# Optimization experiments

Measured on AMD Instinct MI355X. Metric: run time of the kernel, lower is better.

The kernel has to match this reference:

```python
import jax, jax.numpy as jnp
import numpy as np

# Single-directional chamfer distance (pytorch3d semantics):
# chamfer_distance(x, y, single_directional=True) returns
# (mean over batch of mean over points of min_j ||x_i - y_j||^2, None)
# Here forward(v, v_pred) = chamfer_distance(v_pred, v, single_directional=True)

CHUNK = 1024  # tile size over query points to avoid materializing full [B,N,M]

def _min_sqdist(x, y):
    # x: [B, N, 3] queries, y: [B, M, 3] targets
    # returns [B, N] min squared distances, computed in chunks over N
    B, N, D = x.shape
    y_sq = jnp.sum(y * y, axis=-1)  # [B, M]

    def chunk_min(x_chunk):
        # x_chunk: [B, C, 3]
        x_sq = jnp.sum(x_chunk * x_chunk, axis=-1)  # [B, C]
        xy = jnp.einsum('bcd,bmd->bcm', x_chunk, y)  # [B, C, M]
        d2 = x_sq[:, :, None] - 2.0 * xy + y_sq[:, None, :]
        return jnp.min(d2, axis=-1)  # [B, C]

    n_chunks = N // CHUNK
    xr = x.reshape(B, n_chunks, CHUNK, D).transpose(1, 0, 2, 3)  # [n_chunks, B, C, 3]
    mins = jax.lax.map(chunk_min, xr)  # [n_chunks, B, C]
    return mins.transpose(1, 0, 2).reshape(B, N)


def setup_inputs() -> dict:
    key = jax.random.key(0)
    k1, k2 = jax.random.split(key)
    v = jax.random.normal(k1, (8, 16384, 3), dtype=jnp.float32)
    v_pred = jax.random.normal(k2, (8, 16384, 3), dtype=jnp.float32)
    return {"v": v, "v_pred": v_pred}


def reference(v, v_pred):
    # chamfer_distance(v_pred, v, single_directional=True)
    min_d2 = _min_sqdist(v_pred, v)  # [B, N]
    # pytorch3d default: sum over points per cloud, normalize by num points,
    # then mean-reduce over batch (batch_reduction='mean', point_reduction='mean')
    per_cloud = jnp.mean(min_d2, axis=-1)  # [B]
    loss = jnp.sum(per_cloud) / v_pred.shape[0]
    return loss
```

## Files before the change

### kernel.cpp

```cpp
#include <hip/hip_runtime.h>


typedef _Float16 half8 __attribute__((ext_vector_type(8)));
typedef float   f32x16 __attribute__((ext_vector_type(16)));

#define BB 8
#define NN 16384
#define MM 16384
#define THREADS 256
#define WAVES   (THREADS / 64)
#define QT 2
#define Q_PER_BLOCK (WAVES * QT * 32)
#define QC_SPLIT (NN / Q_PER_BLOCK)
#define PASS_TILES 64
#define PASS_TGT  (PASS_TILES * 32)
#define NPASS     (MM / PASS_TGT)

__device__ inline float min3f(float a, float b, float c) {
    return fminf(fminf(a, b), c);
}
__device__ inline float fold16(const f32x16 c, float r) {
    const float t0 = min3f(c[0],  c[1],  c[2]);
    const float t1 = min3f(c[3],  c[4],  c[5]);
    const float t2 = min3f(c[6],  c[7],  c[8]);
    const float t3 = min3f(c[9],  c[10], c[11]);
    const float t4 = min3f(c[12], c[13], c[14]);
    return min3f(min3f(t0, t1, t2), min3f(t3, t4, c[15]), r);
}

__global__ __launch_bounds__(THREADS, 2)
void chamfer_kernel(const float* __restrict__ v,
                    const float* __restrict__ vp,
                    float* __restrict__ out)
{
    __shared__ half8 shA[PASS_TILES * 64];

    const int tid  = threadIdx.x;
    const int lane = tid & 63;
    const int l31  = lane & 31;
    const int hi   = lane >> 5;
    const int wav  = tid >> 6;

    const int bx = blockIdx.x;
    const int qc = bx & (QC_SPLIT - 1);
    const int b  = bx >> 6;

    const float* vb = v  + (size_t)b * MM * 3;
    const float* vq = vp + (size_t)b * NN * 3;

    half8 b0, b1;
    float x20, x21;
    {
        const int qt0 = (qc * Q_PER_BLOCK) / 32 + wav * QT;
#pragma unroll
        for (int j = 0; j < QT; ++j) {
            const int q = (qt0 + j) * 32 + l31;
            const float x = vq[q*3+0], y = vq[q*3+1], z = vq[q*3+2];
            const float hx = (float)(_Float16)x; const float lx = x - hx;
            const float hy = (float)(_Float16)y; const float ly = y - hy;
            const float hz = (float)(_Float16)z; const float lz = z - hz;
            const float x2 = x*x + y*y + z*z;
            half8 t_;
            if (hi == 0) {
                t_[0] = (_Float16)hx; t_[1] = (_Float16)hy; t_[2] = (_Float16)hz;
                t_[3] = (_Float16)(32.f * lx);
                t_[4] = (_Float16)(32.f * ly);
                t_[5] = (_Float16)(32.f * lz);
                t_[6] = (_Float16)(0.03125f * hx);
                t_[7] = (_Float16)(0.03125f * hy);
            } else {
                t_[0] = (_Float16)(0.03125f * hz);
                t_[1] = (_Float16)1.f;
                t_[2] = (_Float16)0.03125f;
                t_[3] = (_Float16)0.f; t_[4] = (_Float16)0.f;
                t_[5] = (_Float16)0.f; t_[6] = (_Float16)0.f; t_[7] = (_Float16)0.f;
            }
            if (j == 0) { b0 = t_; x20 = x2; } else { b1 = t_; x21 = x2; }
        }
    }

    f32x16 Z;
#pragma unroll
    for (int e = 0; e < 16; ++e) Z[e] = 0.f;

    float r0 = 3.4e38f, r1 = 3.4e38f;

    for (int pass = 0; pass < NPASS; ++pass) {
        __syncthreads();
#pragma unroll
        for (int k = 0; k < 8; ++k) {
            const int tl = tid + k * THREADS;
            const int t  = pass * PASS_TGT + tl;
            const float yx = vb[t*3+0], yy = vb[t*3+1], yz = vb[t*3+2];
            const float hx = (float)(_Float16)yx; const float lx = yx - hx;
            const float hy = (float)(_Float16)yy; const float ly = yy - hy;
            const float hz = (float)(_Float16)yz; const float lz = yz - hz;
            const float y2 = yx*yx + yy*yy + yz*yz;
            const float h2 = (float)(_Float16)y2; const float l2 = y2 - h2;
            half8 f0, f1;
            f0[0] = (_Float16)(-2.f     * hx);
            f0[1] = (_Float16)(-2.f     * hy);
            f0[2] = (_Float16)(-2.f     * hz);
            f0[3] = (_Float16)(-0.0625f * hx);
            f0[4] = (_Float16)(-0.0625f * hy);
            f0[5] = (_Float16)(-0.0625f * hz);
            f0[6] = (_Float16)(-64.f    * lx);
            f0[7] = (_Float16)(-64.f    * ly);
            f1[0] = (_Float16)(-64.f    * lz);
            f1[1] = (_Float16)h2;
            f1[2] = (_Float16)(32.f     * l2);
            f1[3] = (_Float16)0.f; f1[4] = (_Float16)0.f;
            f1[5] = (_Float16)0.f; f1[6] = (_Float16)0.f; f1[7] = (_Float16)0.f;
            const int tile = tl >> 5, l = tl & 31;
            shA[tile * 64 + l]      = f0;
            shA[tile * 64 + 32 + l] = f1;
        }
        __syncthreads();

        half8 fA = shA[0 * 64 + lane];
        f32x16 cA0 = __builtin_amdgcn_mfma_f32_32x32x16_f16(fA, b0, Z, 0, 0, 0);
        f32x16 cA1 = __builtin_amdgcn_mfma_f32_32x32x16_f16(fA, b1, Z, 0, 0, 0);
        half8 fB = shA[1 * 64 + lane];

        for (int tt = 0; tt < PASS_TILES - 2; tt += 2) {
            fA = shA[(tt + 2) * 64 + lane];
            const f32x16 cB0 = __builtin_amdgcn_mfma_f32_32x32x16_f16(fB, b0, Z, 0, 0, 0);
            const f32x16 cB1 = __builtin_amdgcn_mfma_f32_32x32x16_f16(fB, b1, Z, 0, 0, 0);
            r0 = fold16(cA0, r0);
            r1 = fold16(cA1, r1);
            fB = shA[(tt + 3) * 64 + lane];
            cA0 = __builtin_amdgcn_mfma_f32_32x32x16_f16(fA, b0, Z, 0, 0, 0);
            cA1 = __builtin_amdgcn_mfma_f32_32x32x16_f16(fA, b1, Z, 0, 0, 0);
            r0 = fold16(cB0, r0);
            r1 = fold16(cB1, r1);
        }
        const f32x16 cB0 = __builtin_amdgcn_mfma_f32_32x32x16_f16(fB, b0, Z, 0, 0, 0);
        const f32x16 cB1 = __builtin_amdgcn_mfma_f32_32x32x16_f16(fB, b1, Z, 0, 0, 0);
        r0 = fold16(cA0, r0);
        r1 = fold16(cA1, r1);
        r0 = fold16(cB0, r0);
        r1 = fold16(cB1, r1);
    }

    const float m0 = fminf(r0, __shfl_xor(r0, 32, 64));
    const float m1 = fminf(r1, __shfl_xor(r1, 32, 64));
    const float d0 = fmaxf(m0 + x20, 0.f);
    const float d1 = fmaxf(m1 + x21, 0.f);
    float s = (hi == 0) ? (d0 + d1) : 0.f;
#pragma unroll
    for (int off = 32; off; off >>= 1) s += __shfl_down(s, off, 64);

    __syncthreads();
    float* fs = (float*)shA;
    if (lane == 0) fs[wav] = s;
    __syncthreads();
    if (tid == 0) {
        const float t = fs[0] + fs[1] + fs[2] + fs[3];
        atomicAdd(out, t * (1.0f / ((float)BB * (float)NN)));
    }
}

extern "C" void kernel_launch(void* const* d_in, const int* in_sizes, int n_in,
                              void* d_out, int out_size, void* d_ws, size_t ws_size,
                              hipStream_t stream) {
    const float* v  = (const float*)d_in[0];
    const float* vp = (const float*)d_in[1];
    float* out = (float*)d_out;

    hipMemsetAsync(out, 0, sizeof(float), stream);
    chamfer_kernel<<<BB * QC_SPLIT, THREADS, 0, stream>>>(v, vp, out);
}
```

Baseline: 128.4 us.

## Precompute target MFMA fragments once and split targets across two wave halves

```diff
diff --git a/kernel.cpp b/kernel.cpp
--- a/kernel.cpp
+++ b/kernel.cpp
@@ -7,14 +7,14 @@
 #define BB 8
 #define NN 16384
 #define MM 16384
-#define THREADS 256
-#define WAVES   (THREADS / 64)
+#define THREADS 512
 #define QT 2
-#define Q_PER_BLOCK (WAVES * QT * 32)
+#define Q_PER_BLOCK 256
 #define QC_SPLIT (NN / Q_PER_BLOCK)
-#define PASS_TILES 64
-#define PASS_TGT  (PASS_TILES * 32)
-#define NPASS     (MM / PASS_TGT)
+#define NPASS 8
+#define HALF_UNITS 2048
+#define WS_UNITS_PER_B 32768
+#define WS_BYTES ((size_t)BB * WS_UNITS_PER_B * 16)
 
 __device__ inline float min3f(float a, float b, float c) {
     return fminf(fminf(a, b), c);
@@ -28,30 +28,68 @@
     return min3f(min3f(t0, t1, t2), min3f(t3, t4, c[15]), r);
 }
 
+__device__ inline void make_frags(float yx, float yy, float yz,
+                                  half8& f0, half8& f1) {
+    const float hx = (float)(_Float16)yx; const float lx = yx - hx;
+    const float hy = (float)(_Float16)yy; const float ly = yy - hy;
+    const float hz = (float)(_Float16)yz; const float lz = yz - hz;
+    const float y2 = yx*yx + yy*yy + yz*yz;
+    const float h2 = (float)(_Float16)y2; const float l2 = y2 - h2;
+    f0[0] = (_Float16)(-2.f     * hx);
+    f0[1] = (_Float16)(-2.f     * hy);
+    f0[2] = (_Float16)(-2.f     * hz);
+    f0[3] = (_Float16)(-0.0625f * hx);
+    f0[4] = (_Float16)(-0.0625f * hy);
+    f0[5] = (_Float16)(-0.0625f * hz);
+    f0[6] = (_Float16)(-64.f    * lx);
+    f0[7] = (_Float16)(-64.f    * ly);
+    f1[0] = (_Float16)(-64.f    * lz);
+    f1[1] = (_Float16)h2;
+    f1[2] = (_Float16)(32.f     * l2);
+    f1[3] = (_Float16)0.f; f1[4] = (_Float16)0.f;
+    f1[5] = (_Float16)0.f; f1[6] = (_Float16)0.f; f1[7] = (_Float16)0.f;
+}
+
+__global__ __launch_bounds__(256)
+void prep_kernel(const float* __restrict__ v, half8* __restrict__ wsf) {
+    const int t  = blockIdx.x * 256 + threadIdx.x;
+    const int b  = t >> 14;
+    const int ti = t & (MM - 1);
+    const float* p = v + (size_t)b * MM * 3 + (size_t)ti * 3;
+    half8 f0, f1;
+    make_frags(p[0], p[1], p[2], f0, f1);
+    const size_t base = (size_t)b * WS_UNITS_PER_B + (size_t)(ti >> 5) * 64 + (ti & 31);
+    wsf[base]      = f0;
+    wsf[base + 32] = f1;
+}
+
+template<int USE_WS>
 __global__ __launch_bounds__(THREADS, 2)
 void chamfer_kernel(const float* __restrict__ v,
                     const float* __restrict__ vp,
+                    const half8* __restrict__ wsf,
                     float* __restrict__ out)
 {
-    __shared__ half8 shA[PASS_TILES * 64];
+    __shared__ half8 shA[2 * HALF_UNITS];
 
     const int tid  = threadIdx.x;
     const int lane = tid & 63;
     const int l31  = lane & 31;
     const int hi   = lane >> 5;
     const int wav  = tid >> 6;
+    const int h    = wav >> 2;
+    const int qw   = wav & 3;
 
     const int bx = blockIdx.x;
     const int qc = bx & (QC_SPLIT - 1);
     const int b  = bx >> 6;
 
-    const float* vb = v  + (size_t)b * MM * 3;
     const float* vq = vp + (size_t)b * NN * 3;
 
     half8 b0, b1;
     float x20, x21;
     {
-        const int qt0 = (qc * Q_PER_BLOCK) / 32 + wav * QT;
+        const int qt0 = qc * (Q_PER_BLOCK / 32) + qw * QT;
 #pragma unroll
         for (int j = 0; j < QT; ++j) {
             const int q = (qt0 + j) * 32 + l31;
@@ -84,78 +122,71 @@
     for (int e = 0; e < 16; ++e) Z[e] = 0.f;
 
     float r0 = 3.4e38f, r1 = 3.4e38f;
+    const half8* tile_base = shA + h * HALF_UNITS;
 
     for (int pass = 0; pass < NPASS; ++pass) {
         __syncthreads();
-#pragma unroll
-        for (int k = 0; k < 8; ++k) {
-            const int tl = tid + k * THREADS;
-            const int t  = pass * PASS_TGT + tl;
-            const float yx = vb[t*3+0], yy = vb[t*3+1], yz = vb[t*3+2];
-            const float hx = (float)(_Float16)yx; const float lx = yx - hx;
-            const float hy = (float)(_Float16)yy; const float ly = yy - hy;
-            const float hz = (float)(_Float16)yz; const float lz = yz - hz;
-            const float y2 = yx*yx + yy*yy + yz*yz;
-            const float h2 = (float)(_Float16)y2; const float l2 = y2 - h2;
-            half8 f0, f1;
-            f0[0] = (_Float16)(-2.f     * hx);
-            f0[1] = (_Float16)(-2.f     * hy);
-            f0[2] = (_Float16)(-2.f     * hz);
-            f0[3] = (_Float16)(-0.0625f * hx);
-            f0[4] = (_Float16)(-0.0625f * hy);
-            f0[5] = (_Float16)(-0.0625f * hz);
-            f0[6] = (_Float16)(-64.f    * lx);
-            f0[7] = (_Float16)(-64.f    * ly);
-            f1[0] = (_Float16)(-64.f    * lz);
-            f1[1] = (_Float16)h2;
-            f1[2] = (_Float16)(32.f     * l2);
-            f1[3] = (_Float16)0.f; f1[4] = (_Float16)0.f;
-            f1[5] = (_Float16)0.f; f1[6] = (_Float16)0.f; f1[7] = (_Float16)0.f;
-            const int tile = tl >> 5, l = tl & 31;
-            shA[tile * 64 + l]      = f0;
-            shA[tile * 64 + 32 + l] = f1;
+        if constexpr (USE_WS) {
+            const uint4* g = (const uint4*)wsf + (size_t)b * WS_UNITS_PER_B;
+            uint4* s = (uint4*)shA;
+#pragma unroll
+            for (int k = 0; k < 4; ++k)
+                s[tid + k * THREADS] = g[pass * 2048 + tid + k * THREADS];
+#pragma unroll
+            for (int k = 0; k < 4; ++k)
+                s[2048 + tid + k * THREADS] = g[16384 + pass * 2048 + tid + k * THREADS];
+        } else {
+            const float* vb = v + (size_t)b * MM * 3;
+#pragma unroll
+            for (int k = 0; k < 4; ++k) {
+                const int tl    = tid + k * THREADS;
+                const int hh    = tl >> 10;
+                const int local = tl & 1023;
+                const int t     = hh * 8192 + pass * 1024 + local;
+                half8 f0, f1;
+                make_frags(vb[t*3+0], vb[t*3+1], vb[t*3+2], f0, f1);
+                const int unit = hh * HALF_UNITS + (local >> 5) * 64 + (local & 31);
+                shA[unit]      = f0;
+                shA[unit + 32] = f1;
+            }
         }
         __syncthreads();
 
-        half8 fA = shA[0 * 64 + lane];
-        f32x16 cA0 = __builtin_amdgcn_mfma_f32_32x32x16_f16(fA, b0, Z, 0, 0, 0);
-        f32x16 cA1 = __builtin_amdgcn_mfma_f32_32x32x16_f16(fA, b1, Z, 0, 0, 0);
-        half8 fB = shA[1 * 64 + lane];
-
-        for (int tt = 0; tt < PASS_TILES - 2; tt += 2) {
-            fA = shA[(tt + 2) * 64 + lane];
-            const f32x16 cB0 = __builtin_amdgcn_mfma_f32_32x32x16_f16(fB, b0, Z, 0, 0, 0);
-            const f32x16 cB1 = __builtin_amdgcn_mfma_f32_32x32x16_f16(fB, b1, Z, 0, 0, 0);
-            r0 = fold16(cA0, r0);
-            r1 = fold16(cA1, r1);
-            fB = shA[(tt + 3) * 64 + lane];
-            cA0 = __builtin_amdgcn_mfma_f32_32x32x16_f16(fA, b0, Z, 0, 0, 0);
-            cA1 = __builtin_amdgcn_mfma_f32_32x32x16_f16(fA, b1, Z, 0, 0, 0);
-            r0 = fold16(cB0, r0);
-            r1 = fold16(cB1, r1);
+        half8 fA = tile_base[lane];
+        for (int tt = 0; tt < 32; tt += 2) {
+            half8 fB = tile_base[(tt + 1) * 64 + lane];
+            f32x16 c0 = __builtin_amdgcn_mfma_f32_32x32x16_f16(fA, b0, Z, 0, 0, 0);
+            f32x16 c1 = __builtin_amdgcn_mfma_f32_32x32x16_f16(fA, b1, Z, 0, 0, 0);
+            r0 = fold16(c0, r0);
+            r1 = fold16(c1, r1);
+            fA = tile_base[(((tt + 2) & 31)) * 64 + lane];
+            c0 = __builtin_amdgcn_mfma_f32_32x32x16_f16(fB, b0, Z, 0, 0, 0);
+            c1 = __builtin_amdgcn_mfma_f32_32x32x16_f16(fB, b1, Z, 0, 0, 0);
+            r0 = fold16(c0, r0);
+            r1 = fold16(c1, r1);
         }
-        const f32x16 cB0 = __builtin_amdgcn_mfma_f32_32x32x16_f16(fB, b0, Z, 0, 0, 0);
-        const f32x16 cB1 = __builtin_amdgcn_mfma_f32_32x32x16_f16(fB, b1, Z, 0, 0, 0);
-        r0 = fold16(cA0, r0);
-        r1 = fold16(cA1, r1);
-        r0 = fold16(cB0, r0);
-        r1 = fold16(cB1, r1);
-    }
-
-    const float m0 = fminf(r0, __shfl_xor(r0, 32, 64));
-    const float m1 = fminf(r1, __shfl_xor(r1, 32, 64));
-    const float d0 = fmaxf(m0 + x20, 0.f);
-    const float d1 = fmaxf(m1 + x21, 0.f);
-    float s = (hi == 0) ? (d0 + d1) : 0.f;
-#pragma unroll
-    for (int off = 32; off; off >>= 1) s += __shfl_down(s, off, 64);
+    }
 
     __syncthreads();
     float* fs = (float*)shA;
-    if (lane == 0) fs[wav] = s;
+    fs[wav * 128 + lane]      = r0;
+    fs[wav * 128 + 64 + lane] = r1;
+    __syncthreads();
+    if (wav < 4) {
+        r0 = fminf(fs[wav * 128 + lane],      fs[(wav + 4) * 128 + lane]);
+        r1 = fminf(fs[wav * 128 + 64 + lane], fs[(wav + 4) * 128 + 64 + lane]);
+        const float m0 = fminf(r0, __shfl_xor(r0, 32, 64));
+        const float m1 = fminf(r1, __shfl_xor(r1, 32, 64));
+        const float d0 = fmaxf(m0 + x20, 0.f);
+        const float d1 = fmaxf(m1 + x21, 0.f);
+        float s = (hi == 0) ? (d0 + d1) : 0.f;
+#pragma unroll
+        for (int off = 32; off; off >>= 1) s += __shfl_down(s, off, 64);
+        if (lane == 0) fs[1024 + wav] = s;
+    }
     __syncthreads();
     if (tid == 0) {
-        const float t = fs[0] + fs[1] + fs[2] + fs[3];
+        const float t = fs[1024] + fs[1025] + fs[1026] + fs[1027];
         atomicAdd(out, t * (1.0f / ((float)BB * (float)NN)));
     }
 }
@@ -168,5 +199,11 @@
     float* out = (float*)d_out;
 
     hipMemsetAsync(out, 0, sizeof(float), stream);
-    chamfer_kernel<<<BB * QC_SPLIT, THREADS, 0, stream>>>(v, vp, out);
-}
+    if (ws_size >= WS_BYTES) {
+        half8* wsf = (half8*)d_ws;
+        prep_kernel<<<(BB * MM) / 256, 256, 0, stream>>>(v, wsf);
+        chamfer_kernel<1><<<BB * QC_SPLIT, THREADS, 0, stream>>>(v, vp, wsf, out);
+    } else {
+        chamfer_kernel<0><<<BB * QC_SPLIT, THREADS, 0, stream>>>(v, vp, nullptr, out);
+    }
+}
```

After: 127.3 us. About the same (-0.8%).
